# Optimization experiments

Hardware: AMD Instinct MI355X
Metric: run time of the kernel (lower is better)

The kernel has to match this reference:

```python
import jax, jax.numpy as jnp
import numpy as np


def setup_inputs() -> dict:
    key = jax.random.key(0)
    ks = jax.random.split(key, 5)
    B, C, S = 4, 64, 96          # batch, in_c, square spatial size
    H = 8                        # num_heads
    x = jax.random.normal(ks[0], (B, C, S, S), dtype=jnp.float32)
    # 1x1 conv weights stored as (out_c, in_c) matrices
    w_vkq = jax.random.normal(ks[1], (3 * H * C, C), dtype=jnp.float32) * 0.02
    b_vkq = jax.random.normal(ks[2], (3 * H * C,), dtype=jnp.float32) * 0.02
    w_out = jax.random.normal(ks[3], (C, C * H), dtype=jnp.float32) * 0.02
    b_out = jax.random.normal(ks[4], (C,), dtype=jnp.float32) * 0.02
    return {"x": x, "w_vkq": w_vkq, "b_vkq": b_vkq, "w_out": w_out, "b_out": b_out}


def reference(x, w_vkq, b_vkq, w_out, b_out):
    B, C, Hh, W = x.shape                       # module requires Hh == W
    H = w_vkq.shape[0] // (3 * C)               # num_heads
    # to_vkq: 1x1 conv == per-pixel matmul over channels -> (B, 3HC, Hh, W)
    vqk = jnp.einsum('bcxy,oc->boxy', x, w_vkq) + b_vkq[None, :, None, None]
    # torch .view reinterprets spatial (Hh, W) flat buffer as (W, Hh)
    vqk = vqk.reshape(B, 3, H, C, W, Hh)
    v, q, k = vqk[:, 0], vqk[:, 1], vqk[:, 2]
    # channel-wise attention: contract over the 'y' axis, keep channel dim
    h = jnp.einsum('bhcxy,bhczy->bhcxz', v, k) / (W * Hh)   # (B,H,C,W,W)
    h = jax.nn.softmax(h, axis=-1)
    h = jnp.einsum('bhcxy,bhczy->bhcxz', h, q)              # (B,H,C,W,W)
    # rearrange 'b h c x y -> b (c h) x y'  (c outer, h inner)
    h = h.transpose(0, 2, 1, 3, 4).reshape(B, C * H, W, W)
    # to_out: 1x1 conv back to in_c channels
    return jnp.einsum('bkxy,ok->boxy', h, w_out) + b_out[None, :, None, None]
```

## Files before the change

kernel.cpp:

```cpp
#include <hip/hip_runtime.h>
#include <cstdint>
#include <cstddef>

typedef float f32x4 __attribute__((ext_vector_type(4)));
typedef float f32x2 __attribute__((ext_vector_type(2)));
typedef __bf16 bf16x8 __attribute__((ext_vector_type(8)));
typedef __bf16 bf16x2 __attribute__((ext_vector_type(2)));
typedef uint32_t u32x4 __attribute__((ext_vector_type(4)));

#define TSS 9216
#define VST 9344
#define VSF 9472
#define KSB 104
#define KST 104
#define XST 72
#define WST 72
#define RSTD 68
#define EPS 68

#define FP8_SCALE 32.0f

__device__ __forceinline__ uint32_t pack2bf(float a, float b) {
  bf16x2 v = { (__bf16)a, (__bf16)b };
  return __builtin_bit_cast(uint32_t, v);
}
__device__ __forceinline__ uint32_t pack4fp8(float a, float b, float c, float d) {
  uint32_t r = __builtin_amdgcn_cvt_pk_fp8_f32(a, b, 0, false);
  return (uint32_t)__builtin_amdgcn_cvt_pk_fp8_f32(c, d, (int)r, true);
}
__device__ __forceinline__ uint2 fp8x4_to_bf16x4_ns(uint32_t v) {
  const f32x2 lo = __builtin_amdgcn_cvt_pk_f32_fp8((int)v, false);
  const f32x2 hi = __builtin_amdgcn_cvt_pk_f32_fp8((int)v, true);
  return uint2{pack2bf(lo[0], lo[1]), pack2bf(hi[0], hi[1])};
}

__global__ __launch_bounds__(256, 8) void wcvt_kernel(
    const float* __restrict__ w_vkq, const float* __restrict__ w_out,
    uint16_t* __restrict__ wbf, uint16_t* __restrict__ wob)
{
  const int i = blockIdx.x * 256 + threadIdx.x;
  if (i < 24576) {
    const float4 v = ((const float4*)w_vkq)[i];
    ((uint2*)wbf)[i] = uint2{pack2bf(v.x * FP8_SCALE, v.y * FP8_SCALE),
                             pack2bf(v.z * FP8_SCALE, v.w * FP8_SCALE)};
  } else {
    const int j = i - 24576;
    const float4 v = ((const float4*)w_out)[j];
    ((uint2*)wob)[j] = uint2{pack2bf(v.x, v.y), pack2bf(v.z, v.w)};
  }
}

__global__ __launch_bounds__(256, 4) void proj_kernel(
    const float* __restrict__ x, const uint16_t* __restrict__ wbf,
    const float* __restrict__ b_vkq,
    uint8_t* __restrict__ Vr, uint8_t* __restrict__ Qr, uint8_t* __restrict__ Kr)
{
  __shared__ __align__(16) uint16_t Bt[64 * XST];
  __shared__ __align__(16) uint8_t  Ep[4][16 * EPS];

  const int t   = threadIdx.x;
  const int blk = blockIdx.x;
  const int oq  = (blk >> 3) & 3;
  const int bn  = (blk & 7) | ((blk >> 5) << 3);
  const int nt  = bn % 144;
  const int b   = bn / 144;
  const int n0  = nt * 64;

  {
    const float* __restrict__ xb = x + (size_t)b * 64 * TSS + n0;
    const int p  = t & 63;
    const int c0 = (t >> 6) * 16;
    float v[16];
    #pragma unroll
    for (int i = 0; i < 16; ++i) v[i] = xb[(size_t)(c0 + i) * TSS + p];
    #pragma unroll
    for (int h = 0; h < 2; ++h)
      *(uint4*)&Bt[p * XST + c0 + h*8] =
        uint4{pack2bf(v[h*8+0], v[h*8+1]), pack2bf(v[h*8+2], v[h*8+3]),
              pack2bf(v[h*8+4], v[h*8+5]), pack2bf(v[h*8+6], v[h*8+7])};
  }
  __syncthreads();

  const int L    = t & 63;
  const int w    = t >> 6;
  const int lcol = L & 15;
  const int lq   = L >> 4;

  bf16x8 af[4][2];
  #pragma unroll
  for (int tm = 0; tm < 4; ++tm)
    #pragma unroll
    for (int ks = 0; ks < 2; ++ks)
      af[tm][ks] = *(const bf16x8*)&Bt[(tm*16 + lcol) * XST + ks*32 + lq*8];

  const int obase = oq * 384 + w * 96;

  bf16x8 bw[3][2];
  float  bias_r[3];
  #pragma unroll
  for (int pre = 0; pre < 3; ++pre) {
    const int o = obase + pre*16 + lcol;
    #pragma unroll
    for (int ks = 0; ks < 2; ++ks)
      bw[pre][ks] = *(const bf16x8*)(wbf + (size_t)o * 64 + ks*32 + lq*8);
    bias_r[pre] = b_vkq[o] * FP8_SCALE;
  }

  uint8_t* __restrict__ ep = Ep[w];

  #pragma unroll
  for (int ot = 0; ot < 6; ++ot) {
    const int s3   = ot % 3;
    const float bias = bias_r[s3];
    f32x4 acc[4];
    #pragma unroll
    for (int tm = 0; tm < 4; ++tm) acc[tm] = f32x4{bias, bias, bias, bias};
    #pragma unroll
    for (int tm = 0; tm < 4; ++tm)
      #pragma unroll
      for (int ks = 0; ks < 2; ++ks)
        acc[tm] = __builtin_amdgcn_mfma_f32_16x16x32_bf16(af[tm][ks], bw[s3][ks], acc[tm], 0, 0, 0);
    if (ot < 3) {
      const int on = obase + (ot + 3)*16 + lcol;
      #pragma unroll
      for (int ks = 0; ks < 2; ++ks)
        bw[s3][ks] = *(const bf16x8*)(wbf + (size_t)on * 64 + ks*32 + lq*8);
      bias_r[s3] = b_vkq[on] * FP8_SCALE;
    }
    #pragma unroll
    for (int tm = 0; tm < 4; ++tm)
      *(uint32_t*)&ep[lcol * EPS + tm*16 + lq*4] =
        pack4fp8(acc[tm][0], acc[tm][1], acc[tm][2], acc[tm][3]);

    const int o_t  = obase + ot * 16;
    const int sreg = o_t >> 9;
    uint8_t* __restrict__ reg = (sreg == 0) ? Vr : ((sreg == 1) ? Qr : Kr);
    const size_t rb = (size_t)(b * 512 + (o_t & 511)) * VSF + n0;
    #pragma unroll
    for (int s = 0; s < 4; ++s) {
      const int orow = s*4 + lq;
      const uint32_t d = *(const uint32_t*)&ep[orow * EPS + lcol*4];
      *(uint32_t*)(reg + rb + (size_t)orow * VSF + lcol*4) = d;
    }
  }
}

__global__ __launch_bounds__(384, 4) void attn_kernel(
    const uint8_t* __restrict__ Vr, const uint8_t* __restrict__ Qr,
    const uint8_t* __restrict__ Kr, uint16_t* __restrict__ Obuf)
{
  __shared__ __align__(16) uint8_t  KP[96 * 208];
  __shared__ __align__(16) uint16_t Qs[96 * KST];

  const int t   = threadIdx.x;
  const int blk = blockIdx.x;
  const int b   = blk >> 9;
  const int hc  = blk & 511;
  const size_t pb8 = (size_t)(b * 512 + hc) * VSF;
  const uint8_t* __restrict__ vplane = Vr + pb8;

  {
    const uint4* __restrict__ sk = (const uint4*)(Kr + pb8);
    const uint4* __restrict__ sq = (const uint4*)(Qr + pb8);
    #pragma unroll
    for (int half = 0; half < 2; ++half) {
      const int g = t + half * 384;
      if (half == 0 || t < 192) {
        const int row = g / 6, seg = g % 6;
        *(uint4*)&KP[row * KSB + seg * 16] = sk[g];
        const uint4 q4 = sq[g];
        const uint2 qa = fp8x4_to_bf16x4_ns(q4.x);
        const uint2 qb = fp8x4_to_bf16x4_ns(q4.y);
        const uint2 qc = fp8x4_to_bf16x4_ns(q4.z);
        const uint2 qd = fp8x4_to_bf16x4_ns(q4.w);
        uint16_t* d = &Qs[row * KST + seg * 16];
        *(uint4*)(d + 0) = uint4{qa.x, qa.y, qb.x, qb.y};
        *(uint4*)(d + 8) = uint4{qc.x, qc.y, qd.x, qd.y};
      }
    }
  }

  const int L    = t & 63;
  const int w    = t / 64;
  const int lcol = L & 15;
  const int lq   = L >> 4;
  const int xrow = 16 * w + lcol;
  const float C  = 1.44269504088896f / (9216.0f * (FP8_SCALE * FP8_SCALE));
  const f32x4 zero4 = {0.f, 0.f, 0.f, 0.f};

  long bv[3];
  #pragma unroll
  for (int ks = 0; ks < 3; ++ks)
    bv[ks] = *(const long*)(vplane + (size_t)xrow * 96 + ks*32 + lq*8);

  __syncthreads();

  f32x4 sa[6];
  #pragma unroll
  for (int i = 0; i < 6; ++i) sa[i] = zero4;
  #pragma unroll
  for (int tz = 0; tz < 6; ++tz)
    #pragma unroll
    for (int ks = 0; ks < 3; ++ks) {
      const long ak = *(const long*)&KP[(tz*16 + lcol) * KSB + ks*32 + lq*8];
      sa[tz] = __builtin_amdgcn_mfma_f32_16x16x32_fp8_fp8(ak, bv[ks], sa[tz], 0, 0, 0);
    }

  float s = 0.f;
  #pragma unroll
  for (int tz = 0; tz < 6; ++tz)
    #pragma unroll
    for (int r = 0; r < 4; ++r) {
      const float e = __builtin_exp2f(sa[tz][r] * C);
      sa[tz][r] = e;
      s += e;
    }
  s += __shfl_xor(s, 16, 64);
  s += __shfl_xor(s, 32, 64);
  const float inv = 1.0f / (s * FP8_SCALE);

  __syncthreads();

  uint16_t* __restrict__ Ps = (uint16_t*)KP;
  #pragma unroll
  for (int tz = 0; tz < 6; ++tz) {
    const float p0 = sa[tz][0] * inv;
    const float p1 = sa[tz][1] * inv;
    const float p2 = sa[tz][2] * inv;
    const float p3 = sa[tz][3] * inv;
    *(uint2*)&Ps[xrow * KST + tz*16 + lq*4] = uint2{pack2bf(p0, p1), pack2bf(p2, p3)};
  }

  bf16x8 bp[3];
  #pragma unroll
  for (int ks = 0; ks < 3; ++ks)
    bp[ks] = *(const bf16x8*)&Ps[xrow * KST + ks*32 + lq*8];
  f32x4 oa[6];
  #pragma unroll
  for (int i = 0; i < 6; ++i) oa[i] = zero4;
  #pragma unroll
  for (int tz = 0; tz < 6; ++tz)
    #pragma unroll
    for (int ks = 0; ks < 3; ++ks) {
      const bf16x8 aq = *(const bf16x8*)&Qs[(tz*16 + lcol) * KST + ks*32 + lq*8];
      oa[tz] = __builtin_amdgcn_mfma_f32_16x16x32_bf16(aq, bp[ks], oa[tz], 0, 0, 0);
    }

  uint16_t* __restrict__ dst = Obuf + (size_t)(b * 512 + hc) * VST;
  #pragma unroll
  for (int tz = 0; tz < 6; ++tz)
    *(uint2*)(dst + (size_t)xrow * 96 + tz*16 + lq*4) =
      uint2{pack2bf(oa[tz][0], oa[tz][1]), pack2bf(oa[tz][2], oa[tz][3])};
}

__global__ __launch_bounds__(512, 4) void out_proj_kernel(
    const uint16_t* __restrict__ Obuf, const uint16_t* __restrict__ wob,
    const float* __restrict__ b_out, float* __restrict__ out)
{
  __shared__ __align__(16) uint32_t As2[2][32 * RSTD];
  __shared__ __align__(16) uint16_t Wl[2][64 * WST];

  const int t    = threadIdx.x;
  const int blk  = blockIdx.x;
  const int nt   = blk % 144;
  const int b    = blk / 144;
  const int n0   = nt * 64;
  const int L    = t & 63;
  const int w    = t >> 6;
  const int wo   = w >> 1;
  const int wp   = w & 1;
  const int lcol = L & 15;
  const int lq   = L >> 4;
  const int kp_g = t >> 4;
  const int seg  = t & 15;

  const uint16_t* __restrict__ ab = Obuf + (size_t)b * 512 * VST;

  uint2 pa[2];
  uint2 pwb[2];

  auto load_chunk = [&](int k0) {
    const int ke = k0 + 2*kp_g, ko = ke + 1;
    const int pe = ((ke & 7) << 6) | (ke >> 3);
    const int po = ((ko & 7) << 6) | (ko >> 3);
    pa[0] = *(const uint2*)(ab + (size_t)pe * VST + n0 + seg * 4);
    pa[1] = *(const uint2*)(ab + (size_t)po * VST + n0 + seg * 4);
    #pragma unroll
    for (int i = 0; i < 2; ++i) {
      const int idx = t + i * 512;
      pwb[i] = *(const uint2*)(wob + (size_t)(idx >> 4) * 512 + k0 + (idx & 15) * 4);
    }
  };

  auto store_chunk = [&](int buf) {
    {
      const uint2 a = pa[0], bb = pa[1];
      uint4 d;
      d.x = (a.x & 0xffffu) | (bb.x << 16);
      d.y = (a.x >> 16)     | (bb.x & 0xffff0000u);
      d.z = (a.y & 0xffffu) | (bb.y << 16);
      d.w = (a.y >> 16)     | (bb.y & 0xffff0000u);
      *(uint4*)&As2[buf][kp_g * RSTD + seg * 4] = d;
    }
    #pragma unroll
    for (int i = 0; i < 2; ++i) {
      const int idx = t + i * 512;
      *(uint2*)&Wl[buf][(idx >> 4) * WST + (idx & 15) * 4] = pwb[i];
    }
  };

  f32x4 acc[2];
  const f32x4 zero4 = {0.f, 0.f, 0.f, 0.f};
  #pragma unroll
  for (int tm = 0; tm < 2; ++tm) acc[tm] = zero4;

  load_chunk(0);

  for (int c = 0; c < 8; ++c) {
    const int buf = c & 1;
    store_chunk(buf);
    if (c < 7) load_chunk((c + 1) * 64);
    __syncthreads();
    #pragma unroll
    for (int ks = 0; ks < 2; ++ks) {
      const bf16x8 af = *(const bf16x8*)&Wl[buf][(wo*16 + lcol) * WST + ks*32 + lq*8];
      #pragma unroll
      for (int tm = 0; tm < 2; ++tm) {
        u32x4 bb;
        #pragma unroll
        for (int jj = 0; jj < 4; ++jj)
          bb[jj] = As2[buf][(ks*16 + lq*4 + jj) * RSTD + (wp*2 + tm)*16 + lcol];
        const bf16x8 bfr = __builtin_bit_cast(bf16x8, bb);
        acc[tm] = __builtin_amdgcn_mfma_f32_16x16x32_bf16(af, bfr, acc[tm], 0, 0, 0);
      }
    }
  }

  #pragma unroll
  for (int tm = 0; tm < 2; ++tm) {
    const int p = n0 + (wp*2 + tm)*16 + lcol;
    #pragma unroll
    for (int r = 0; r < 4; ++r) {
      const int o = wo*16 + lq*4 + r;
      out[(size_t)(b * 64 + o) * TSS + p] = acc[tm][r] + b_out[o];
    }
  }
}

extern "C" void kernel_launch(void* const* d_in, const int* in_sizes, int n_in,
                              void* d_out, int out_size, void* d_ws, size_t ws_size,
                              hipStream_t stream) {
  const float* x     = (const float*)d_in[0];
  const float* w_vkq = (const float*)d_in[1];
  const float* b_vkq = (const float*)d_in[2];
  const float* w_out = (const float*)d_in[3];
  const float* b_out = (const float*)d_in[4];
  float* out = (float*)d_out;

  uint16_t* Obuf = (uint16_t*)d_ws;
  uint8_t*  Vr   = (uint8_t*)(Obuf + (size_t)2048 * VST);
  uint8_t*  Qr   = Vr + (size_t)2048 * VSF;
  uint8_t*  Kr   = Qr + (size_t)2048 * VSF;
  uint16_t* wbf  = (uint16_t*)(Kr + (size_t)2048 * VSF);
  uint16_t* wob  = wbf + (size_t)98304;

  wcvt_kernel<<<dim3(128), dim3(256), 0, stream>>>(w_vkq, w_out, wbf, wob);
  proj_kernel<<<dim3(2304), dim3(256), 0, stream>>>(x, wbf, b_vkq, Vr, Qr, Kr);
  attn_kernel<<<dim3(2048), dim3(384), 0, stream>>>(Vr, Qr, Kr, Obuf);
  out_proj_kernel<<<dim3(576), dim3(512), 0, stream>>>(Obuf, wob, b_out, out);
}
```

Before: 120.6 us.

## Keep Q as fp8 in shared memory and convert at MFMA load time

```diff
diff --git a/kernel.cpp b/kernel.cpp
--- a/kernel.cpp
+++ b/kernel.cpp
@@ -11,8 +11,6 @@
 #define TSS 9216
 #define VST 9344
 #define VSF 9472
-#define KSB 104
-#define KST 104
 #define XST 72
 #define WST 72
 #define RSTD 68
@@ -149,8 +147,7 @@
     const uint8_t* __restrict__ Vr, const uint8_t* __restrict__ Qr,
     const uint8_t* __restrict__ Kr, uint16_t* __restrict__ Obuf)
 {
-  __shared__ __align__(16) uint8_t  KP[96 * 208];
-  __shared__ __align__(16) uint16_t Qs[96 * KST];
+  __shared__ __align__(16) uint8_t KQ[29952];
 
   const int t   = threadIdx.x;
   const int blk = blockIdx.x;
@@ -159,25 +156,19 @@
   const size_t pb8 = (size_t)(b * 512 + hc) * VSF;
   const uint8_t* __restrict__ vplane = Vr + pb8;
 
-  {
-    const uint4* __restrict__ sk = (const uint4*)(Kr + pb8);
-    const uint4* __restrict__ sq = (const uint4*)(Qr + pb8);
-    #pragma unroll
-    for (int half = 0; half < 2; ++half) {
-      const int g = t + half * 384;
-      if (half == 0 || t < 192) {
-        const int row = g / 6, seg = g % 6;
-        *(uint4*)&KP[row * KSB + seg * 16] = sk[g];
-        const uint4 q4 = sq[g];
-        const uint2 qa = fp8x4_to_bf16x4_ns(q4.x);
-        const uint2 qb = fp8x4_to_bf16x4_ns(q4.y);
-        const uint2 qc = fp8x4_to_bf16x4_ns(q4.z);
-        const uint2 qd = fp8x4_to_bf16x4_ns(q4.w);
-        uint16_t* d = &Qs[row * KST + seg * 16];
-        *(uint4*)(d + 0) = uint4{qa.x, qa.y, qb.x, qb.y};
-        *(uint4*)(d + 8) = uint4{qc.x, qc.y, qd.x, qd.y};
-      }
-    }
+  const uint4* __restrict__ sk = (const uint4*)(Kr + pb8);
+  const uint4* __restrict__ sq = (const uint4*)(Qr + pb8);
+
+  uint4 q0, q1;
+  const int r0 = t / 6, s0 = t % 6;
+  int r1 = 0, s1 = 0;
+  q0 = sq[t];
+  *(uint4*)&KQ[9984 + r0 * 104 + s0 * 16] = sk[t];
+  if (t < 192) {
+    const int g = t + 384;
+    r1 = g / 6; s1 = g % 6;
+    q1 = sq[g];
+    *(uint4*)&KQ[9984 + r1 * 104 + s1 * 16] = sk[g];
   }
 
   const int L    = t & 63;
@@ -202,9 +193,13 @@
   for (int tz = 0; tz < 6; ++tz)
     #pragma unroll
     for (int ks = 0; ks < 3; ++ks) {
-      const long ak = *(const long*)&KP[(tz*16 + lcol) * KSB + ks*32 + lq*8];
+      const long ak = *(const long*)&KQ[9984 + (tz*16 + lcol) * 104 + ks*32 + lq*8];
       sa[tz] = __builtin_amdgcn_mfma_f32_16x16x32_fp8_fp8(ak, bv[ks], sa[tz], 0, 0, 0);
     }
+
+  *(uint4*)&KQ[r0 * 104 + s0 * 16] = q0;
+  if (t < 192)
+    *(uint4*)&KQ[r1 * 104 + s1 * 16] = q1;
 
   float s = 0.f;
   #pragma unroll
@@ -221,20 +216,19 @@
 
   __syncthreads();
 
-  uint16_t* __restrict__ Ps = (uint16_t*)KP;
   #pragma unroll
   for (int tz = 0; tz < 6; ++tz) {
     const float p0 = sa[tz][0] * inv;
     const float p1 = sa[tz][1] * inv;
     const float p2 = sa[tz][2] * inv;
     const float p3 = sa[tz][3] * inv;
-    *(uint2*)&Ps[xrow * KST + tz*16 + lq*4] = uint2{pack2bf(p0, p1), pack2bf(p2, p3)};
+    *(uint2*)&KQ[9984 + xrow * 208 + tz*32 + lq*8] = uint2{pack2bf(p0, p1), pack2bf(p2, p3)};
   }
 
   bf16x8 bp[3];
   #pragma unroll
   for (int ks = 0; ks < 3; ++ks)
-    bp[ks] = *(const bf16x8*)&Ps[xrow * KST + ks*32 + lq*8];
+    bp[ks] = *(const bf16x8*)&KQ[9984 + xrow * 208 + ks*64 + lq*16];
   f32x4 oa[6];
   #pragma unroll
   for (int i = 0; i < 6; ++i) oa[i] = zero4;
@@ -242,7 +236,10 @@
   for (int tz = 0; tz < 6; ++tz)
     #pragma unroll
     for (int ks = 0; ks < 3; ++ks) {
-      const bf16x8 aq = *(const bf16x8*)&Qs[(tz*16 + lcol) * KST + ks*32 + lq*8];
+      const uint2 qraw = *(const uint2*)&KQ[(tz*16 + lcol) * 104 + ks*32 + lq*8];
+      const uint2 a0 = fp8x4_to_bf16x4_ns(qraw.x);
+      const uint2 a1 = fp8x4_to_bf16x4_ns(qraw.y);
+      const bf16x8 aq = __builtin_bit_cast(bf16x8, uint4{a0.x, a0.y, a1.x, a1.y});
       oa[tz] = __builtin_amdgcn_mfma_f32_16x16x32_bf16(aq, bp[ks], oa[tz], 0, 0, 0);
     }
 
```

After: 120.4 us, median of 2. No clear change (-0.2%).
